# Performance work log

Hardware: AMD Instinct MI355X
Metric: run time of the kernel (lower is better)

The kernel has to match this reference:

```python
import jax, jax.numpy as jnp
import numpy as np

E = 1024   # embd_size
H = 16     # heads_num
DH = E // H
DFF = 4 * E
B, T = 2, 2048


def layer_norm(x, g, b, eps=1e-5):
    mu = jnp.mean(x, axis=-1, keepdims=True)
    var = jnp.var(x, axis=-1, keepdims=True)
    return (x - mu) * jax.lax.rsqrt(var + eps) * g + b


def setup_inputs() -> dict:
    key = jax.random.key(0)
    ks = jax.random.split(key, 12)
    s = 0.02
    return {
        "x": jax.random.normal(ks[0], (B, T, E), dtype=jnp.float32),
        "Wq": jax.random.normal(ks[1], (E, E), dtype=jnp.float32) * s,
        "Wk": jax.random.normal(ks[2], (E, E), dtype=jnp.float32) * s,
        "Wv": jax.random.normal(ks[3], (E, E), dtype=jnp.float32) * s,
        "Wo": jax.random.normal(ks[4], (E, E), dtype=jnp.float32) * s,
        "bo": jnp.zeros((E,), dtype=jnp.float32),
        "W1": jax.random.normal(ks[5], (E, DFF), dtype=jnp.float32) * s,
        "b1": jnp.zeros((DFF,), dtype=jnp.float32),
        "W2": jax.random.normal(ks[6], (DFF, E), dtype=jnp.float32) * s,
        "b2": jnp.zeros((E,), dtype=jnp.float32),
        "g1": jnp.ones((E,), dtype=jnp.float32),
        "be1": jnp.zeros((E,), dtype=jnp.float32),
        "g2": jnp.ones((E,), dtype=jnp.float32),
        "be2": jnp.zeros((E,), dtype=jnp.float32),
    }


def reference(x, Wq, Wk, Wv, Wo, bo, W1, b1, W2, b2, g1, be1, g2, be2):
    Bx, Tx, C = x.shape
    # --- self-attention sublayer ---
    h = layer_norm(x, g1, be1)
    # per-head projections; heads concatenated along output dim == stacked weights
    q = (h @ Wq).reshape(Bx, Tx, H, DH)  # [B,T,H,Dh]
    k = (h @ Wk).reshape(Bx, Tx, H, DH)
    v = (h @ Wv).reshape(Bx, Tx, H, DH)
    # NOTE: original scales by full embd_size**-0.5 (C = x.shape[-1]), not head_size
    scale = C ** (-0.5)
    scores = jnp.einsum("bqhd,bkhd->bhqk", q, k) * scale  # [B,H,T,T]
    mask = jnp.tril(jnp.ones((Tx, Tx), dtype=bool))
    scores = jnp.where(mask, scores, -jnp.inf)
    attn = jax.nn.softmax(scores, axis=-1)
    o = jnp.einsum("bhqk,bkhd->bqhd", attn, v).reshape(Bx, Tx, C)
    sa = o @ Wo + bo
    x = x + sa
    # --- feed-forward sublayer ---
    h2 = layer_norm(x, g2, be2)
    ff = jax.nn.relu(h2 @ W1 + b1) @ W2 + b2
    return x + ff
```

## Files before the change

### kernel.cpp

```cpp
#include <hip/hip_runtime.h>
#include <hip/hip_bf16.h>
#include <math.h>

#define Bn 2
#define Tn 2048
#define En 1024
#define Hn 16
#define DFFn 4096
#define Mn (Bn*Tn)
#define QKVLD 3072

typedef __hip_bfloat16 bf16;
typedef unsigned short u16;
typedef __attribute__((ext_vector_type(8))) short short8;
typedef __attribute__((ext_vector_type(4))) float f32x4;

typedef __attribute__((address_space(1))) const void cg_void;
typedef __attribute__((address_space(3))) void lds_void;

#define HBAR() asm volatile("s_waitcnt lgkmcnt(0)\n\ts_barrier" ::: "memory")

__device__ __forceinline__ u16 f2bf(float f) {
    bf16 h = __float2bfloat16(f);
    u16 u; __builtin_memcpy(&u, &h, 2); return u;
}

__global__ __launch_bounds__(256)
void transpose_w4(const float* __restrict__ s0, const float* __restrict__ s1,
                  const float* __restrict__ s2, const float* __restrict__ s3,
                  u16* __restrict__ d0, u16* __restrict__ d1,
                  u16* __restrict__ d2, u16* __restrict__ d3) {
    const float* src = (blockIdx.z == 0) ? s0 : (blockIdx.z == 1) ? s1
                     : (blockIdx.z == 2) ? s2 : s3;
    u16* dst = (blockIdx.z == 0) ? d0 : (blockIdx.z == 1) ? d1
             : (blockIdx.z == 2) ? d2 : d3;
    __shared__ float t[64][65];
    const int r0 = blockIdx.y * 64, c0 = blockIdx.x * 64;
    const int tr = threadIdx.x >> 6, tc = threadIdx.x & 63;
#pragma unroll
    for (int i = 0; i < 16; i++)
        t[tr + i * 4][tc] = src[(size_t)(r0 + tr + i * 4) * 1024 + c0 + tc];
    __syncthreads();
#pragma unroll
    for (int i = 0; i < 16; i++)
        dst[(size_t)(c0 + tr + i * 4) * 1024 + r0 + tc] = f2bf(t[tc][tr + i * 4]);
}

__global__ __launch_bounds__(256)
void transpose_w(const float* __restrict__ src, u16* __restrict__ dst,
                 int R, int C) {
    __shared__ float t[64][65];
    const int r0 = blockIdx.y * 64, c0 = blockIdx.x * 64;
    const int tr = threadIdx.x >> 6, tc = threadIdx.x & 63;
#pragma unroll
    for (int i = 0; i < 16; i++)
        t[tr + i * 4][tc] = src[(size_t)(r0 + tr + i * 4) * C + c0 + tc];
    __syncthreads();
#pragma unroll
    for (int i = 0; i < 16; i++)
        dst[(size_t)(c0 + tr + i * 4) * R + r0 + tc] = f2bf(t[tc][tr + i * 4]);
}

__global__ __launch_bounds__(256)
void ln_kernel(const float* __restrict__ x, const float* __restrict__ g,
               const float* __restrict__ b, u16* __restrict__ out) {
    const int row = blockIdx.x;
    const int tid = threadIdx.x;
    const float* xp = x + (size_t)row * En;
    float v[4];
    float s = 0.f, sq = 0.f;
#pragma unroll
    for (int i = 0; i < 4; i++) {
        v[i] = xp[tid + i * 256];
        s += v[i];
        sq += v[i] * v[i];
    }
    __shared__ float rs[256], rq[256];
    rs[tid] = s; rq[tid] = sq;
    __syncthreads();
    for (int st = 128; st > 0; st >>= 1) {
        if (tid < st) { rs[tid] += rs[tid + st]; rq[tid] += rq[tid + st]; }
        __syncthreads();
    }
    const float mu  = rs[0] * (1.0f / En);
    const float var = rq[0] * (1.0f / En) - mu * mu;
    const float inv = rsqrtf(var + 1e-5f);
#pragma unroll
    for (int i = 0; i < 4; i++) {
        const int c = tid + i * 256;
        out[(size_t)row * En + c] = f2bf((v[i] - mu) * inv * g[c] + b[c]);
    }
}

template<int TM, int HAS_BIAS, int RELU, int HAS_RES, int OUT_F32>
__global__ __launch_bounds__(256)
void gemm_bt(const u16* __restrict__ A, int ldA,
             const u16* __restrict__ Wt, int ldW,
             const float* __restrict__ bias, const float* __restrict__ res,
             void* __restrict__ Cout, int ldC, int Kd) {
    constexpr int IF = TM / 32;
    __shared__ __align__(16) u16 As[TM * 32];
    __shared__ __align__(16) u16 Bs[128 * 32];
    const int tid  = threadIdx.x;
    const int lane = tid & 63, wv = tid >> 6;
    const int quad = lane >> 4, l16 = lane & 15;
    const int m0 = blockIdx.y * TM, n0 = blockIdx.x * 128;
    const int rw = (wv >> 1) * (TM / 2), cw = (wv & 1) * 64;
    const int lr  = lane >> 2;
    const int gsw = ((lane & 3) ^ ((lane >> 3) & 3)) * 8;
    const int psw = (quad ^ ((l16 >> 1) & 3)) * 8;

    f32x4 acc[IF][4] = {};

    for (int kt = 0; kt < Kd; kt += 32) {
        __syncthreads();
#pragma unroll
        for (int t = 0; t < TM / 64; t++) {
            const int row = wv * (TM / 4) + t * 16;
            __builtin_amdgcn_global_load_lds(
                (cg_void*)(const void*)&A[(size_t)(m0 + row + lr) * ldA + kt + gsw],
                (lds_void*)(void*)&As[row * 32], 16, 0, 0);
        }
#pragma unroll
        for (int t = 0; t < 2; t++) {
            const int row = wv * 32 + t * 16;
            __builtin_amdgcn_global_load_lds(
                (cg_void*)(const void*)&Wt[(size_t)(n0 + row + lr) * ldW + kt + gsw],
                (lds_void*)(void*)&Bs[row * 32], 16, 0, 0);
        }
        __syncthreads();

        short8 af[IF], bfr[4];
#pragma unroll
        for (int i = 0; i < IF; i++)
            af[i] = *(const short8*)&As[(rw + i * 16 + l16) * 32 + psw];
#pragma unroll
        for (int j = 0; j < 4; j++)
            bfr[j] = *(const short8*)&Bs[(cw + j * 16 + l16) * 32 + psw];
#pragma unroll
        for (int i = 0; i < IF; i++)
#pragma unroll
            for (int j = 0; j < 4; j++)
                acc[i][j] = __builtin_amdgcn_mfma_f32_16x16x32_bf16(
                    af[i], bfr[j], acc[i][j], 0, 0, 0);
    }

#pragma unroll
    for (int i = 0; i < IF; i++) {
#pragma unroll
        for (int r = 0; r < 4; r++) {
            const int gm = m0 + rw + i * 16 + quad * 4 + r;
#pragma unroll
            for (int j = 0; j < 4; j++) {
                const int gn = n0 + cw + j * 16 + l16;
                float c = acc[i][j][r];
                if (HAS_BIAS) c += bias[gn];
                if (RELU) c = fmaxf(c, 0.f);
                if (HAS_RES) c += res[(size_t)gm * ldC + gn];
                if (OUT_F32) ((float*)Cout)[(size_t)gm * ldC + gn] = c;
                else         ((u16*)Cout)[(size_t)gm * ldC + gn] = f2bf(c);
            }
        }
    }
}

__global__ __launch_bounds__(256)
void flash_attn(u16* __restrict__ QKV) {
    const int hh = blockIdx.y, bb = blockIdx.z;
    const int tid  = threadIdx.x;
    const int lane = tid & 63, wv = tid >> 6;
    const int quad = lane >> 4, l16 = lane & 15;

    __shared__ __align__(16) u16 Qs[64 * 88];
    __shared__ __align__(16) u16 Ks[2][64 * 88];
    __shared__ __align__(16) u16 Vt[2][64 * 88];
    __shared__ __align__(16) u16 Ps[4][16 * 70];

    const size_t rowbase = (size_t)(bb * Tn) * QKVLD;
    const int sr = tid >> 2, scg = tid & 3;
    const int vkey = tid & 63, vw = tid >> 6;
    const float SC = 0.03125f * 1.44269504089f;

    for (int qsel = 0; qsel < 2; qsel++) {
        const int qt = qsel ? (31 - blockIdx.x) : blockIdx.x;

        HBAR();
        {
            const size_t qb = rowbase + (size_t)(qt * 64 + sr) * QKVLD + hh * 64;
            *(uint4*)&Qs[sr * 88 + scg * 8]       = *(const uint4*)&QKV[qb + scg * 8];
            *(uint4*)&Qs[sr * 88 + (scg + 4) * 8] = *(const uint4*)&QKV[qb + (scg + 4) * 8];
        }
        uint4 kreg0, kreg1, vreg0, vreg1;
        {
            const size_t kb = rowbase + (size_t)sr * QKVLD + 1024 + hh * 64;
            kreg0 = *(const uint4*)&QKV[kb + scg * 8];
            kreg1 = *(const uint4*)&QKV[kb + (scg + 4) * 8];
            const size_t vb = rowbase + (size_t)vkey * QKVLD + 2048 + hh * 64 + vw * 16;
            vreg0 = *(const uint4*)&QKV[vb];
            vreg1 = *(const uint4*)&QKV[vb + 8];
            *(uint4*)&Ks[0][sr * 88 + scg * 8]       = kreg0;
            *(uint4*)&Ks[0][sr * 88 + (scg + 4) * 8] = kreg1;
            u16 vtmp[16];
            *(uint4*)&vtmp[0] = vreg0;
            *(uint4*)&vtmp[8] = vreg1;
#pragma unroll
            for (int u = 0; u < 16; u++)
                Vt[0][(vw * 16 + u) * 88 + vkey] = vtmp[u];
        }
        if (qt >= 1) {
            const size_t kb = rowbase + (size_t)(64 + sr) * QKVLD + 1024 + hh * 64;
            kreg0 = *(const uint4*)&QKV[kb + scg * 8];
            kreg1 = *(const uint4*)&QKV[kb + (scg + 4) * 8];
            const size_t vb = rowbase + (size_t)(64 + vkey) * QKVLD + 2048 + hh * 64 + vw * 16;
            vreg0 = *(const uint4*)&QKV[vb];
            vreg1 = *(const uint4*)&QKV[vb + 8];
        }
        HBAR();
        short8 qf[2];
        qf[0] = *(const short8*)&Qs[(wv * 16 + l16) * 88 + quad * 8];
        qf[1] = *(const short8*)&Qs[(wv * 16 + l16) * 88 + 32 + quad * 8];

        f32x4 ot[4] = {};
        float m2 = -INFINITY, lrow = 0.f;

        for (int kt = 0; kt <= qt; kt++) {
            const int cur = kt & 1;

            f32x4 st[4] = {};
#pragma unroll
            for (int ks = 0; ks < 2; ks++)
#pragma unroll
                for (int i = 0; i < 4; i++) {
                    short8 kf = *(const short8*)&Ks[cur][(i * 16 + l16) * 88 + ks * 32 + quad * 8];
                    st[i] = __builtin_amdgcn_mfma_f32_16x16x32_bf16(kf, qf[ks], st[i], 0, 0, 0);
                }

            float p[4][4];
            float tmax = -INFINITY;
            if (kt == qt) {
                const int qloc = wv * 16 + l16;
#pragma unroll
                for (int i = 0; i < 4; i++)
#pragma unroll
                    for (int r = 0; r < 4; r++) {
                        float s = st[i][r] * SC;
                        if (i * 16 + quad * 4 + r > qloc) s = -INFINITY;
                        p[i][r] = s;
                        tmax = fmaxf(tmax, s);
                    }
            } else {
#pragma unroll
                for (int i = 0; i < 4; i++)
#pragma unroll
                    for (int r = 0; r < 4; r++) {
                        const float s = st[i][r] * SC;
                        p[i][r] = s;
                        tmax = fmaxf(tmax, s);
                    }
            }
            tmax = fmaxf(tmax, __shfl_xor(tmax, 16));
            tmax = fmaxf(tmax, __shfl_xor(tmax, 32));

            const float mnew = fmaxf(m2, tmax);
            const float alpha = exp2f(m2 - mnew);
            m2 = mnew;
            float psum = 0.f;
#pragma unroll
            for (int i = 0; i < 4; i++)
#pragma unroll
                for (int r = 0; r < 4; r++) {
                    const float e = exp2f(p[i][r] - mnew);
                    p[i][r] = e;
                    psum += e;
                }
            psum += __shfl_xor(psum, 16);
            psum += __shfl_xor(psum, 32);
            lrow = lrow * alpha + psum;
#pragma unroll
            for (int i = 0; i < 4; i++) ot[i] *= alpha;

#pragma unroll
            for (int i = 0; i < 4; i++)
#pragma unroll
                for (int r = 0; r < 4; r++)
                    Ps[wv][l16 * 70 + i * 16 + quad * 4 + r] = f2bf(p[i][r]);
            asm volatile("s_waitcnt lgkmcnt(0)" ::: "memory");

#pragma unroll
            for (int ks = 0; ks < 2; ks++) {
                short8 pf = *(const short8*)&Ps[wv][l16 * 70 + ks * 32 + quad * 8];
#pragma unroll
                for (int i = 0; i < 4; i++) {
                    short8 vf = *(const short8*)&Vt[cur][(i * 16 + l16) * 88 + ks * 32 + quad * 8];
                    ot[i] = __builtin_amdgcn_mfma_f32_16x16x32_bf16(vf, pf, ot[i], 0, 0, 0);
                }
            }

            if (kt < qt) {
                *(uint4*)&Ks[cur ^ 1][sr * 88 + scg * 8]       = kreg0;
                *(uint4*)&Ks[cur ^ 1][sr * 88 + (scg + 4) * 8] = kreg1;
                u16 vtmp[16];
                *(uint4*)&vtmp[0] = vreg0;
                *(uint4*)&vtmp[8] = vreg1;
#pragma unroll
                for (int u = 0; u < 16; u++)
                    Vt[cur ^ 1][(vw * 16 + u) * 88 + vkey] = vtmp[u];
                if (kt + 1 < qt) {
                    const size_t kb = rowbase + (size_t)((kt + 2) * 64 + sr) * QKVLD + 1024 + hh * 64;
                    kreg0 = *(const uint4*)&QKV[kb + scg * 8];
                    kreg1 = *(const uint4*)&QKV[kb + (scg + 4) * 8];
                    const size_t vb = rowbase + (size_t)((kt + 2) * 64 + vkey) * QKVLD + 2048 + hh * 64 + vw * 16;
                    vreg0 = *(const uint4*)&QKV[vb];
                    vreg1 = *(const uint4*)&QKV[vb + 8];
                }
                HBAR();
            }
        }

        const float linv = 1.0f / lrow;
        const size_t obase = rowbase + (size_t)(qt * 64 + wv * 16 + l16) * QKVLD + hh * 64;
#pragma unroll
        for (int i = 0; i < 4; i++) {
            ushort4 o4;
            o4.x = f2bf(ot[i][0] * linv);
            o4.y = f2bf(ot[i][1] * linv);
            o4.z = f2bf(ot[i][2] * linv);
            o4.w = f2bf(ot[i][3] * linv);
            *(ushort4*)&QKV[obase + i * 16 + quad * 4] = o4;
        }
    }
}

extern "C" void kernel_launch(void* const* d_in, const int* in_sizes, int n_in,
                              void* d_out, int out_size, void* d_ws, size_t ws_size,
                              hipStream_t stream) {
    const float* x   = (const float*)d_in[0];
    const float* Wq  = (const float*)d_in[1];
    const float* Wk  = (const float*)d_in[2];
    const float* Wv  = (const float*)d_in[3];
    const float* Wo  = (const float*)d_in[4];
    const float* bo  = (const float*)d_in[5];
    const float* W1  = (const float*)d_in[6];
    const float* b1  = (const float*)d_in[7];
    const float* W2  = (const float*)d_in[8];
    const float* b2  = (const float*)d_in[9];
    const float* g1  = (const float*)d_in[10];
    const float* be1 = (const float*)d_in[11];
    const float* g2  = (const float*)d_in[12];
    const float* be2 = (const float*)d_in[13];

    char* wsb = (char*)d_ws;
    u16*   QKV = (u16*)wsb;
    u16*   F1  = (u16*)wsb;
    u16*   W2T = (u16*)(wsb + 16u * 1024 * 1024);
    float* X1  = (float*)(wsb + 24u * 1024 * 1024);
    u16*   h     = (u16*)d_out;
    u16*   WT    = (u16*)((char*)d_out + 8u * 1024 * 1024);
    u16*   WqkvT = WT;
    u16*   WoT   = WT + 3u * 1024 * 1024;
    u16*   W1T   = WT;

    transpose_w4<<<dim3(16, 16, 4), 256, 0, stream>>>(
        Wq, Wk, Wv, Wo,
        WqkvT, WqkvT + 1024u * 1024, WqkvT + 2048u * 1024, WoT);

    ln_kernel<<<Mn, 256, 0, stream>>>(x, g1, be1, h);

    gemm_bt<128, 0, 0, 0, 0><<<dim3(24, 32), 256, 0, stream>>>(
        h, En, WqkvT, En, nullptr, nullptr, QKV, QKVLD, En);

    flash_attn<<<dim3(16, Hn, Bn), 256, 0, stream>>>(QKV);

    gemm_bt<64, 1, 0, 1, 1><<<dim3(8, 64), 256, 0, stream>>>(
        QKV, QKVLD, WoT, En, bo, x, X1, En, En);

    transpose_w<<<dim3(64, 16), 256, 0, stream>>>(W1, W1T, 1024, 4096);
    transpose_w<<<dim3(16, 64), 256, 0, stream>>>(W2, W2T, 4096, 1024);

    ln_kernel<<<Mn, 256, 0, stream>>>(X1, g2, be2, h);

    gemm_bt<128, 1, 1, 0, 0><<<dim3(16, 32), 256, 0, stream>>>(
        h, En, W1T, En, b1, nullptr, F1, 2048, En);
    gemm_bt<64, 0, 0, 1, 1><<<dim3(8, 64), 256, 0, stream>>>(
        F1, 2048, W2T, DFFn, nullptr, X1, X1, En, 2048);
    gemm_bt<128, 1, 1, 0, 0><<<dim3(16, 32), 256, 0, stream>>>(
        h, En, W1T + 2048u * 1024, En, b1 + 2048, nullptr, F1, 2048, En);
    gemm_bt<64, 1, 0, 1, 1><<<dim3(8, 64), 256, 0, stream>>>(
        F1, 2048, W2T + 2048, DFFn, b2, X1, (float*)d_out, En, 2048);
}
```

Baseline: 393.9 us.

## Use 128-key attention tiles and fold softmax scale into Q projection

The flash attention loop now processes 128 keys per round instead of 64, with a 64-key tail round for even query tiles. This halves the number of barriers and online-softmax rescales per query tile. Q fragments are loaded straight from global memory instead of being staged through LDS, and V is transposed with packed 32-bit LDS writes. The softmax scale times log2(e) is applied in the QKV GEMM epilogue before Q is rounded to bf16, which removes the per-score multiply but changes rounding slightly. Single buffering of K/V with register prefetch replaces the double-buffered LDS.

```diff
diff --git a/kernel.cpp b/kernel.cpp
--- a/kernel.cpp
+++ b/kernel.cpp
@@ -12,11 +12,14 @@
 
 typedef __hip_bfloat16 bf16;
 typedef unsigned short u16;
+typedef unsigned int u32;
 typedef __attribute__((ext_vector_type(8))) short short8;
 typedef __attribute__((ext_vector_type(4))) float f32x4;
 
 typedef __attribute__((address_space(1))) const void cg_void;
 typedef __attribute__((address_space(3))) void lds_void;
+
+#define QSC 0.0450842200278f
 
 #define HBAR() asm volatile("s_waitcnt lgkmcnt(0)\n\ts_barrier" ::: "memory")
 
@@ -92,7 +95,7 @@
     }
 }
 
-template<int TM, int HAS_BIAS, int RELU, int HAS_RES, int OUT_F32>
+template<int TM, int HAS_BIAS, int RELU, int HAS_RES, int OUT_F32, int SCQ>
 __global__ __launch_bounds__(256)
 void gemm_bt(const u16* __restrict__ A, int ldA,
              const u16* __restrict__ Wt, int ldW,
@@ -145,6 +148,7 @@
                     af[i], bfr[j], acc[i][j], 0, 0, 0);
     }
 
+    const float qscale = (SCQ && n0 < 1024) ? QSC : 1.0f;
 #pragma unroll
     for (int i = 0; i < IF; i++) {
 #pragma unroll
@@ -157,9 +161,73 @@
                 if (HAS_BIAS) c += bias[gn];
                 if (RELU) c = fmaxf(c, 0.f);
                 if (HAS_RES) c += res[(size_t)gm * ldC + gn];
+                if (SCQ) c *= qscale;
                 if (OUT_F32) ((float*)Cout)[(size_t)gm * ldC + gn] = c;
                 else         ((u16*)Cout)[(size_t)gm * ldC + gn] = f2bf(c);
             }
+        }
+    }
+}
+
+template<int NI, bool MASK>
+__device__ __forceinline__ void attn_round(
+    const u16* __restrict__ Ks, const u16* __restrict__ Vt,
+    u16* __restrict__ Psw, const short8* qf, f32x4* ot,
+    float& m2, float& lrow, int quad, int l16, int qloc) {
+    f32x4 st[NI];
+#pragma unroll
+    for (int i = 0; i < NI; i++) st[i] = (f32x4){0.f, 0.f, 0.f, 0.f};
+#pragma unroll
+    for (int ks = 0; ks < 2; ks++)
+#pragma unroll
+        for (int i = 0; i < NI; i++) {
+            short8 kf = *(const short8*)&Ks[(i * 16 + l16) * 72 + ks * 32 + quad * 8];
+            st[i] = __builtin_amdgcn_mfma_f32_16x16x32_bf16(kf, qf[ks], st[i], 0, 0, 0);
+        }
+    float tmax = -INFINITY;
+#pragma unroll
+    for (int i = 0; i < NI; i++)
+#pragma unroll
+        for (int r = 0; r < 4; r++) {
+            float s = st[i][r];
+            if (MASK && (i * 16 + quad * 4 + r > qloc)) s = -INFINITY;
+            st[i][r] = s;
+            tmax = fmaxf(tmax, s);
+        }
+    tmax = fmaxf(tmax, __shfl_xor(tmax, 16));
+    tmax = fmaxf(tmax, __shfl_xor(tmax, 32));
+    const float mnew = fmaxf(m2, tmax);
+    const float alpha = exp2f(m2 - mnew);
+    m2 = mnew;
+    float psum = 0.f;
+#pragma unroll
+    for (int i = 0; i < NI; i++)
+#pragma unroll
+        for (int r = 0; r < 4; r++) {
+            const float e = exp2f(st[i][r] - mnew);
+            st[i][r] = e;
+            psum += e;
+        }
+    psum += __shfl_xor(psum, 16);
+    psum += __shfl_xor(psum, 32);
+    lrow = lrow * alpha + psum;
+#pragma unroll
+    for (int i = 0; i < 4; i++) ot[i] *= alpha;
+#pragma unroll
+    for (int i = 0; i < NI; i++) {
+        uint2 w;
+        w.x = (u32)f2bf(st[i][0]) | ((u32)f2bf(st[i][1]) << 16);
+        w.y = (u32)f2bf(st[i][2]) | ((u32)f2bf(st[i][3]) << 16);
+        *(uint2*)&Psw[l16 * 136 + i * 16 + quad * 4] = w;
+    }
+    asm volatile("s_waitcnt lgkmcnt(0)" ::: "memory");
+#pragma unroll
+    for (int ks = 0; ks < NI / 2; ks++) {
+        short8 pf = *(const short8*)&Psw[l16 * 136 + ks * 32 + quad * 8];
+#pragma unroll
+        for (int i = 0; i < 4; i++) {
+            short8 vf = *(const short8*)&Vt[(i * 16 + l16) * 136 + ks * 32 + quad * 8];
+            ot[i] = __builtin_amdgcn_mfma_f32_16x16x32_bf16(vf, pf, ot[i], 0, 0, 0);
         }
     }
 }
@@ -171,154 +239,109 @@
     const int lane = tid & 63, wv = tid >> 6;
     const int quad = lane >> 4, l16 = lane & 15;
 
-    __shared__ __align__(16) u16 Qs[64 * 88];
-    __shared__ __align__(16) u16 Ks[2][64 * 88];
-    __shared__ __align__(16) u16 Vt[2][64 * 88];
-    __shared__ __align__(16) u16 Ps[4][16 * 70];
+    __shared__ __align__(16) u16 Ks[128 * 72];
+    __shared__ __align__(16) u16 Vt[64 * 136];
+    __shared__ __align__(16) u16 Ps[4][16 * 136];
 
     const size_t rowbase = (size_t)(bb * Tn) * QKVLD;
-    const int sr = tid >> 2, scg = tid & 3;
-    const int vkey = tid & 63, vw = tid >> 6;
-    const float SC = 0.03125f * 1.44269504089f;
+    const int k_r = tid >> 1, k_g = tid & 1;
+    const int v_kk = (tid & 63) * 2, v_dh = wv * 16;
+    const int k64_r = tid >> 2, k64_g = tid & 3;
+    const int v64_kk = (tid & 31) * 2, v64_dh = (tid >> 5) * 8;
+
+    uint4 kr0, kr1, kr2, kr3, vr0, vr1, vr2, vr3;
+
+    auto prefetch128 = [&](int kb) {
+        const size_t kbb = rowbase + (size_t)(kb + k_r) * QKVLD + 1024 + hh * 64;
+        kr0 = *(const uint4*)&QKV[kbb + k_g * 8];
+        kr1 = *(const uint4*)&QKV[kbb + (k_g + 2) * 8];
+        kr2 = *(const uint4*)&QKV[kbb + (k_g + 4) * 8];
+        kr3 = *(const uint4*)&QKV[kbb + (k_g + 6) * 8];
+        const size_t vb0 = rowbase + (size_t)(kb + v_kk) * QKVLD + 2048 + hh * 64 + v_dh;
+        vr0 = *(const uint4*)&QKV[vb0];
+        vr1 = *(const uint4*)&QKV[vb0 + 8];
+        vr2 = *(const uint4*)&QKV[vb0 + QKVLD];
+        vr3 = *(const uint4*)&QKV[vb0 + QKVLD + 8];
+    };
+    auto write128 = [&]() {
+        *(uint4*)&Ks[k_r * 72 + k_g * 8]       = kr0;
+        *(uint4*)&Ks[k_r * 72 + (k_g + 2) * 8] = kr1;
+        *(uint4*)&Ks[k_r * 72 + (k_g + 4) * 8] = kr2;
+        *(uint4*)&Ks[k_r * 72 + (k_g + 6) * 8] = kr3;
+        u16 va[16], vb[16];
+        *(uint4*)&va[0] = vr0; *(uint4*)&va[8] = vr1;
+        *(uint4*)&vb[0] = vr2; *(uint4*)&vb[8] = vr3;
+#pragma unroll
+        for (int j = 0; j < 16; j++) {
+            const u32 w = (u32)va[j] | ((u32)vb[j] << 16);
+            *(u32*)&Vt[(v_dh + j) * 136 + v_kk] = w;
+        }
+    };
+    auto stage64 = [&](int kb) {
+        const size_t kbb = rowbase + (size_t)(kb + k64_r) * QKVLD + 1024 + hh * 64;
+        *(uint4*)&Ks[k64_r * 72 + k64_g * 8]       = *(const uint4*)&QKV[kbb + k64_g * 8];
+        *(uint4*)&Ks[k64_r * 72 + (k64_g + 4) * 8] = *(const uint4*)&QKV[kbb + (k64_g + 4) * 8];
+        const size_t vb0 = rowbase + (size_t)(kb + v64_kk) * QKVLD + 2048 + hh * 64 + v64_dh;
+        uint4 p0 = *(const uint4*)&QKV[vb0];
+        uint4 p1 = *(const uint4*)&QKV[vb0 + QKVLD];
+        u16 pa[8], pb[8];
+        *(uint4*)&pa[0] = p0; *(uint4*)&pb[0] = p1;
+#pragma unroll
+        for (int j = 0; j < 8; j++) {
+            const u32 w = (u32)pa[j] | ((u32)pb[j] << 16);
+            *(u32*)&Vt[(v64_dh + j) * 136 + v64_kk] = w;
+        }
+    };
 
     for (int qsel = 0; qsel < 2; qsel++) {
         const int qt = qsel ? (31 - blockIdx.x) : blockIdx.x;
-
-        HBAR();
-        {
-            const size_t qb = rowbase + (size_t)(qt * 64 + sr) * QKVLD + hh * 64;
-            *(uint4*)&Qs[sr * 88 + scg * 8]       = *(const uint4*)&QKV[qb + scg * 8];
-            *(uint4*)&Qs[sr * 88 + (scg + 4) * 8] = *(const uint4*)&QKV[qb + (scg + 4) * 8];
-        }
-        uint4 kreg0, kreg1, vreg0, vreg1;
-        {
-            const size_t kb = rowbase + (size_t)sr * QKVLD + 1024 + hh * 64;
-            kreg0 = *(const uint4*)&QKV[kb + scg * 8];
-            kreg1 = *(const uint4*)&QKV[kb + (scg + 4) * 8];
-            const size_t vb = rowbase + (size_t)vkey * QKVLD + 2048 + hh * 64 + vw * 16;
-            vreg0 = *(const uint4*)&QKV[vb];
-            vreg1 = *(const uint4*)&QKV[vb + 8];
-            *(uint4*)&Ks[0][sr * 88 + scg * 8]       = kreg0;
-            *(uint4*)&Ks[0][sr * 88 + (scg + 4) * 8] = kreg1;
-            u16 vtmp[16];
-            *(uint4*)&vtmp[0] = vreg0;
-            *(uint4*)&vtmp[8] = vreg1;
-#pragma unroll
-            for (int u = 0; u < 16; u++)
-                Vt[0][(vw * 16 + u) * 88 + vkey] = vtmp[u];
-        }
-        if (qt >= 1) {
-            const size_t kb = rowbase + (size_t)(64 + sr) * QKVLD + 1024 + hh * 64;
-            kreg0 = *(const uint4*)&QKV[kb + scg * 8];
-            kreg1 = *(const uint4*)&QKV[kb + (scg + 4) * 8];
-            const size_t vb = rowbase + (size_t)(64 + vkey) * QKVLD + 2048 + hh * 64 + vw * 16;
-            vreg0 = *(const uint4*)&QKV[vb];
-            vreg1 = *(const uint4*)&QKV[vb + 8];
-        }
-        HBAR();
+        const int n128 = (qt >> 1) + (qt & 1);
+        const int qloc16 = wv * 16 + l16;
+
+        const size_t qrow = rowbase + (size_t)(qt * 64 + qloc16) * QKVLD + hh * 64;
         short8 qf[2];
-        qf[0] = *(const short8*)&Qs[(wv * 16 + l16) * 88 + quad * 8];
-        qf[1] = *(const short8*)&Qs[(wv * 16 + l16) * 88 + 32 + quad * 8];
+        qf[0] = *(const short8*)&QKV[qrow + quad * 8];
+        qf[1] = *(const short8*)&QKV[qrow + 32 + quad * 8];
 
         f32x4 ot[4] = {};
         float m2 = -INFINITY, lrow = 0.f;
 
-        for (int kt = 0; kt <= qt; kt++) {
-            const int cur = kt & 1;
-
-            f32x4 st[4] = {};
-#pragma unroll
-            for (int ks = 0; ks < 2; ks++)
-#pragma unroll
-                for (int i = 0; i < 4; i++) {
-                    short8 kf = *(const short8*)&Ks[cur][(i * 16 + l16) * 88 + ks * 32 + quad * 8];
-                    st[i] = __builtin_amdgcn_mfma_f32_16x16x32_bf16(kf, qf[ks], st[i], 0, 0, 0);
-                }
-
-            float p[4][4];
-            float tmax = -INFINITY;
-            if (kt == qt) {
-                const int qloc = wv * 16 + l16;
-#pragma unroll
-                for (int i = 0; i < 4; i++)
-#pragma unroll
-                    for (int r = 0; r < 4; r++) {
-                        float s = st[i][r] * SC;
-                        if (i * 16 + quad * 4 + r > qloc) s = -INFINITY;
-                        p[i][r] = s;
-                        tmax = fmaxf(tmax, s);
-                    }
-            } else {
-#pragma unroll
-                for (int i = 0; i < 4; i++)
-#pragma unroll
-                    for (int r = 0; r < 4; r++) {
-                        const float s = st[i][r] * SC;
-                        p[i][r] = s;
-                        tmax = fmaxf(tmax, s);
-                    }
-            }
-            tmax = fmaxf(tmax, __shfl_xor(tmax, 16));
-            tmax = fmaxf(tmax, __shfl_xor(tmax, 32));
-
-            const float mnew = fmaxf(m2, tmax);
-            const float alpha = exp2f(m2 - mnew);
-            m2 = mnew;
-            float psum = 0.f;
-#pragma unroll
-            for (int i = 0; i < 4; i++)
-#pragma unroll
-                for (int r = 0; r < 4; r++) {
-                    const float e = exp2f(p[i][r] - mnew);
-                    p[i][r] = e;
-                    psum += e;
-                }
-            psum += __shfl_xor(psum, 16);
-            psum += __shfl_xor(psum, 32);
-            lrow = lrow * alpha + psum;
-#pragma unroll
-            for (int i = 0; i < 4; i++) ot[i] *= alpha;
-
-#pragma unroll
-            for (int i = 0; i < 4; i++)
-#pragma unroll
-                for (int r = 0; r < 4; r++)
-                    Ps[wv][l16 * 70 + i * 16 + quad * 4 + r] = f2bf(p[i][r]);
-            asm volatile("s_waitcnt lgkmcnt(0)" ::: "memory");
-
-#pragma unroll
-            for (int ks = 0; ks < 2; ks++) {
-                short8 pf = *(const short8*)&Ps[wv][l16 * 70 + ks * 32 + quad * 8];
-#pragma unroll
-                for (int i = 0; i < 4; i++) {
-                    short8 vf = *(const short8*)&Vt[cur][(i * 16 + l16) * 88 + ks * 32 + quad * 8];
-                    ot[i] = __builtin_amdgcn_mfma_f32_16x16x32_bf16(vf, pf, ot[i], 0, 0, 0);
+        HBAR();
+        if (n128 > 0) {
+            prefetch128(0);
+            write128();
+            if (n128 > 1) prefetch128(128);
+            HBAR();
+            for (int f = 0; f < n128; f++) {
+                const bool maskthis = (qt & 1) && (f == n128 - 1);
+                if (maskthis)
+                    attn_round<8, true>(Ks, Vt, &Ps[wv][0], qf, ot, m2, lrow,
+                                        quad, l16, qloc16 + 64);
+                else
+                    attn_round<8, false>(Ks, Vt, &Ps[wv][0], qf, ot, m2, lrow,
+                                         quad, l16, 0);
+                HBAR();
+                if (f + 1 < n128) {
+                    write128();
+                    if (f + 2 < n128) prefetch128((f + 2) * 128);
+                    HBAR();
+                } else if (!(qt & 1)) {
+                    stage64(qt * 64);
+                    HBAR();
                 }
             }
-
-            if (kt < qt) {
-                *(uint4*)&Ks[cur ^ 1][sr * 88 + scg * 8]       = kreg0;
-                *(uint4*)&Ks[cur ^ 1][sr * 88 + (scg + 4) * 8] = kreg1;
-                u16 vtmp[16];
-                *(uint4*)&vtmp[0] = vreg0;
-                *(uint4*)&vtmp[8] = vreg1;
-#pragma unroll
-                for (int u = 0; u < 16; u++)
-                    Vt[cur ^ 1][(vw * 16 + u) * 88 + vkey] = vtmp[u];
-                if (kt + 1 < qt) {
-                    const size_t kb = rowbase + (size_t)((kt + 2) * 64 + sr) * QKVLD + 1024 + hh * 64;
-                    kreg0 = *(const uint4*)&QKV[kb + scg * 8];
-                    kreg1 = *(const uint4*)&QKV[kb + (scg + 4) * 8];
-                    const size_t vb = rowbase + (size_t)((kt + 2) * 64 + vkey) * QKVLD + 2048 + hh * 64 + vw * 16;
-                    vreg0 = *(const uint4*)&QKV[vb];
-                    vreg1 = *(const uint4*)&QKV[vb + 8];
-                }
-                HBAR();
-            }
+            if (!(qt & 1))
+                attn_round<4, true>(Ks, Vt, &Ps[wv][0], qf, ot, m2, lrow,
+                                    quad, l16, qloc16);
+        } else {
+            stage64(0);
+            HBAR();
+            attn_round<4, true>(Ks, Vt, &Ps[wv][0], qf, ot, m2, lrow,
+                                quad, l16, qloc16);
         }
 
         const float linv = 1.0f / lrow;
-        const size_t obase = rowbase + (size_t)(qt * 64 + wv * 16 + l16) * QKVLD + hh * 64;
+        const size_t obase = rowbase + (size_t)(qt * 64 + qloc16) * QKVLD + hh * 64;
 #pragma unroll
         for (int i = 0; i < 4; i++) {
             ushort4 o4;
@@ -366,12 +389,12 @@
 
     ln_kernel<<<Mn, 256, 0, stream>>>(x, g1, be1, h);
 
-    gemm_bt<128, 0, 0, 0, 0><<<dim3(24, 32), 256, 0, stream>>>(
+    gemm_bt<128, 0, 0, 0, 0, 1><<<dim3(24, 32), 256, 0, stream>>>(
         h, En, WqkvT, En, nullptr, nullptr, QKV, QKVLD, En);
 
     flash_attn<<<dim3(16, Hn, Bn), 256, 0, stream>>>(QKV);
 
-    gemm_bt<64, 1, 0, 1, 1><<<dim3(8, 64), 256, 0, stream>>>(
+    gemm_bt<64, 1, 0, 1, 1, 0><<<dim3(8, 64), 256, 0, stream>>>(
         QKV, QKVLD, WoT, En, bo, x, X1, En, En);
 
     transpose_w<<<dim3(64, 16), 256, 0, stream>>>(W1, W1T, 1024, 4096);
@@ -379,12 +402,12 @@
 
     ln_kernel<<<Mn, 256, 0, stream>>>(X1, g2, be2, h);
 
-    gemm_bt<128, 1, 1, 0, 0><<<dim3(16, 32), 256, 0, stream>>>(
+    gemm_bt<128, 1, 1, 0, 0, 0><<<dim3(16, 32), 256, 0, stream>>>(
         h, En, W1T, En, b1, nullptr, F1, 2048, En);
-    gemm_bt<64, 0, 0, 1, 1><<<dim3(8, 64), 256, 0, stream>>>(
+    gemm_bt<64, 0, 0, 1, 1, 0><<<dim3(8, 64), 256, 0, stream>>>(
         F1, 2048, W2T, DFFn, nullptr, X1, X1, En, 2048);
-    gemm_bt<128, 1, 1, 0, 0><<<dim3(16, 32), 256, 0, stream>>>(
+    gemm_bt<128, 1, 1, 0, 0, 0><<<dim3(16, 32), 256, 0, stream>>>(
         h, En, W1T + 2048u * 1024, En, b1 + 2048, nullptr, F1, 2048, En);
-    gemm_bt<64, 1, 0, 1, 1><<<dim3(8, 64), 256, 0, stream>>>(
+    gemm_bt<64, 1, 0, 1, 1, 0><<<dim3(8, 64), 256, 0, stream>>>(
         F1, 2048, W2T + 2048, DFFn, b2, X1, (float*)d_out, En, 2048);
 }
```

Result: no change. 399.8 us (+1.5%).

## Split causal attention across two KV halves with merge pass and pre-transposed V

Applied to the files above, without the earlier changes.

Splits each query tile's key range into two interleaved halves handled by separate blocks, doubling the attention grid, and merges the partial outputs in a new kernel using saved max and sum statistics. V is pre-transposed into a separate buffer by a new kernel, so flash blocks load it with vector loads instead of scalar LDS transposes. LDS tiles use XOR swizzling instead of padding, and the softmax scale is folded into the Q projection epilogue. The residual X1 is also stored as bf16 instead of fp32 to cut traffic. These add extra kernel launches and bf16 rounding of partial outputs and the residual, which may cost accuracy.

```diff
diff --git a/kernel.cpp b/kernel.cpp
--- a/kernel.cpp
+++ b/kernel.cpp
@@ -12,17 +12,23 @@
 
 typedef __hip_bfloat16 bf16;
 typedef unsigned short u16;
+typedef unsigned int u32;
 typedef __attribute__((ext_vector_type(8))) short short8;
 typedef __attribute__((ext_vector_type(4))) float f32x4;
 
 typedef __attribute__((address_space(1))) const void cg_void;
 typedef __attribute__((address_space(3))) void lds_void;
+
+#define QSC 0.0450842200278f
 
 #define HBAR() asm volatile("s_waitcnt lgkmcnt(0)\n\ts_barrier" ::: "memory")
 
 __device__ __forceinline__ u16 f2bf(float f) {
     bf16 h = __float2bfloat16(f);
     u16 u; __builtin_memcpy(&u, &h, 2); return u;
+}
+__device__ __forceinline__ float bf2f(u16 u) {
+    u32 x = ((u32)u) << 16; float f; __builtin_memcpy(&f, &x, 4); return f;
 }
 
 __global__ __launch_bounds__(256)
@@ -62,16 +68,35 @@
 }
 
 __global__ __launch_bounds__(256)
-void ln_kernel(const float* __restrict__ x, const float* __restrict__ g,
+void vcopy_t(const u16* __restrict__ QKV, u16* __restrict__ Vg) {
+    const int bh = blockIdx.z;
+    const int t0 = blockIdx.y * 64;
+    __shared__ u16 t[64][65];
+    const int tr = threadIdx.x >> 6, tc = threadIdx.x & 63;
+    const u16* src = QKV + (size_t)(bh >> 4) * 2048 * QKVLD + 2048 + (bh & 15) * 64;
+#pragma unroll
+    for (int i = 0; i < 16; i++)
+        t[tr + i * 4][tc] = src[(size_t)(t0 + tr + i * 4) * QKVLD + tc];
+    __syncthreads();
+    u16* dst = Vg + (size_t)bh * 64 * 2048;
+#pragma unroll
+    for (int i = 0; i < 16; i++)
+        dst[(size_t)(tr + i * 4) * 2048 + t0 + tc] = t[tc][tr + i * 4];
+}
+
+template<typename AT>
+__global__ __launch_bounds__(256)
+void ln_kernel(const AT* __restrict__ x, const float* __restrict__ g,
                const float* __restrict__ b, u16* __restrict__ out) {
     const int row = blockIdx.x;
     const int tid = threadIdx.x;
-    const float* xp = x + (size_t)row * En;
+    const AT* xp = x + (size_t)row * En;
     float v[4];
     float s = 0.f, sq = 0.f;
 #pragma unroll
     for (int i = 0; i < 4; i++) {
-        v[i] = xp[tid + i * 256];
+        if constexpr (sizeof(AT) == 2) v[i] = bf2f(xp[tid + i * 256]);
+        else                           v[i] = (float)xp[tid + i * 256];
         s += v[i];
         sq += v[i] * v[i];
     }
@@ -92,11 +117,11 @@
     }
 }
 
-template<int TM, int HAS_BIAS, int RELU, int HAS_RES, int OUT_F32>
+template<int TM, int HAS_BIAS, int RELU, int RES, int OUT_F32, int SCQ>
 __global__ __launch_bounds__(256)
 void gemm_bt(const u16* __restrict__ A, int ldA,
              const u16* __restrict__ Wt, int ldW,
-             const float* __restrict__ bias, const float* __restrict__ res,
+             const float* __restrict__ bias, const void* __restrict__ res,
              void* __restrict__ Cout, int ldC, int Kd) {
     constexpr int IF = TM / 32;
     __shared__ __align__(16) u16 As[TM * 32];
@@ -145,6 +170,7 @@
                     af[i], bfr[j], acc[i][j], 0, 0, 0);
     }
 
+    const float qscale = (SCQ && n0 < 1024) ? QSC : 1.0f;
 #pragma unroll
     for (int i = 0; i < IF; i++) {
 #pragma unroll
@@ -156,7 +182,9 @@
                 float c = acc[i][j][r];
                 if (HAS_BIAS) c += bias[gn];
                 if (RELU) c = fmaxf(c, 0.f);
-                if (HAS_RES) c += res[(size_t)gm * ldC + gn];
+                if (RES == 1) c += ((const float*)res)[(size_t)gm * ldC + gn];
+                if (RES == 2) c += bf2f(((const u16*)res)[(size_t)gm * ldC + gn]);
+                if (SCQ) c *= qscale;
                 if (OUT_F32) ((float*)Cout)[(size_t)gm * ldC + gn] = c;
                 else         ((u16*)Cout)[(size_t)gm * ldC + gn] = f2bf(c);
             }
@@ -165,170 +193,199 @@
 }
 
 __global__ __launch_bounds__(256)
-void flash_attn(u16* __restrict__ QKV) {
+void flash_pass1(const u16* __restrict__ QKV, const u16* __restrict__ Vg,
+                 u16* __restrict__ Op0, u16* __restrict__ Op1qkv,
+                 float* __restrict__ stats) {
+    const int pr = blockIdx.x >> 1, half = blockIdx.x & 1;
     const int hh = blockIdx.y, bb = blockIdx.z;
     const int tid  = threadIdx.x;
     const int lane = tid & 63, wv = tid >> 6;
     const int quad = lane >> 4, l16 = lane & 15;
 
-    __shared__ __align__(16) u16 Qs[64 * 88];
-    __shared__ __align__(16) u16 Ks[2][64 * 88];
-    __shared__ __align__(16) u16 Vt[2][64 * 88];
-    __shared__ __align__(16) u16 Ps[4][16 * 70];
+    __shared__ __align__(16) u16 Ks[2][64 * 64];
+    __shared__ __align__(16) u16 Vt[2][64 * 64];
+    __shared__ __align__(16) u16 Ps[4][16 * 64];
 
     const size_t rowbase = (size_t)(bb * Tn) * QKVLD;
-    const int sr = tid >> 2, scg = tid & 3;
-    const int vkey = tid & 63, vw = tid >> 6;
-    const float SC = 0.03125f * 1.44269504089f;
+    const u16* Vgh = Vg + (size_t)(bb * Hn + hh) * 64 * 2048;
+
+    const int sr = tid >> 2;
+    const int p0 = (tid & 3) | ((sr & 1) << 2);
+    const int p1 = p0 ^ 4;
+    const int g0 = p0 ^ (sr & 7), g1 = p1 ^ (sr & 7);
+    const int lsw = l16 & 7;
+
+    uint4 kA, kB, vA, vB;
+    auto prefetch = [&](int kt) {
+        const size_t kb = rowbase + (size_t)(kt * 64 + sr) * QKVLD + 1024 + hh * 64;
+        kA = *(const uint4*)&QKV[kb + g0 * 8];
+        kB = *(const uint4*)&QKV[kb + g1 * 8];
+        const size_t vb = (size_t)sr * 2048 + kt * 64;
+        vA = *(const uint4*)&Vgh[vb + g0 * 8];
+        vB = *(const uint4*)&Vgh[vb + g1 * 8];
+    };
+    auto writebuf = [&](int buf) {
+        *(uint4*)&Ks[buf][sr * 64 + p0 * 8] = kA;
+        *(uint4*)&Ks[buf][sr * 64 + p1 * 8] = kB;
+        *(uint4*)&Vt[buf][sr * 64 + p0 * 8] = vA;
+        *(uint4*)&Vt[buf][sr * 64 + p1 * 8] = vB;
+    };
 
     for (int qsel = 0; qsel < 2; qsel++) {
-        const int qt = qsel ? (31 - blockIdx.x) : blockIdx.x;
-
-        HBAR();
-        {
-            const size_t qb = rowbase + (size_t)(qt * 64 + sr) * QKVLD + hh * 64;
-            *(uint4*)&Qs[sr * 88 + scg * 8]       = *(const uint4*)&QKV[qb + scg * 8];
-            *(uint4*)&Qs[sr * 88 + (scg + 4) * 8] = *(const uint4*)&QKV[qb + (scg + 4) * 8];
-        }
-        uint4 kreg0, kreg1, vreg0, vreg1;
-        {
-            const size_t kb = rowbase + (size_t)sr * QKVLD + 1024 + hh * 64;
-            kreg0 = *(const uint4*)&QKV[kb + scg * 8];
-            kreg1 = *(const uint4*)&QKV[kb + (scg + 4) * 8];
-            const size_t vb = rowbase + (size_t)vkey * QKVLD + 2048 + hh * 64 + vw * 16;
-            vreg0 = *(const uint4*)&QKV[vb];
-            vreg1 = *(const uint4*)&QKV[vb + 8];
-            *(uint4*)&Ks[0][sr * 88 + scg * 8]       = kreg0;
-            *(uint4*)&Ks[0][sr * 88 + (scg + 4) * 8] = kreg1;
-            u16 vtmp[16];
-            *(uint4*)&vtmp[0] = vreg0;
-            *(uint4*)&vtmp[8] = vreg1;
-#pragma unroll
-            for (int u = 0; u < 16; u++)
-                Vt[0][(vw * 16 + u) * 88 + vkey] = vtmp[u];
-        }
-        if (qt >= 1) {
-            const size_t kb = rowbase + (size_t)(64 + sr) * QKVLD + 1024 + hh * 64;
-            kreg0 = *(const uint4*)&QKV[kb + scg * 8];
-            kreg1 = *(const uint4*)&QKV[kb + (scg + 4) * 8];
-            const size_t vb = rowbase + (size_t)(64 + vkey) * QKVLD + 2048 + hh * 64 + vw * 16;
-            vreg0 = *(const uint4*)&QKV[vb];
-            vreg1 = *(const uint4*)&QKV[vb + 8];
-        }
-        HBAR();
-        short8 qf[2];
-        qf[0] = *(const short8*)&Qs[(wv * 16 + l16) * 88 + quad * 8];
-        qf[1] = *(const short8*)&Qs[(wv * 16 + l16) * 88 + 32 + quad * 8];
+        const int qt = qsel ? (31 - pr) : pr;
+        const int nk = (qt >= half) ? ((qt - half) >> 1) + 1 : 0;
+        const int qrow = qt * 64 + wv * 16 + l16;
+        const int grow = bb * Tn + qrow;
 
         f32x4 ot[4] = {};
         float m2 = -INFINITY, lrow = 0.f;
 
-        for (int kt = 0; kt <= qt; kt++) {
-            const int cur = kt & 1;
-
-            f32x4 st[4] = {};
-#pragma unroll
-            for (int ks = 0; ks < 2; ks++)
+        HBAR();
+        if (nk > 0) {
+            const u16* qp = QKV + rowbase + (size_t)qrow * QKVLD + hh * 64;
+            short8 qf[2];
+            qf[0] = *(const short8*)&qp[quad * 8];
+            qf[1] = *(const short8*)&qp[32 + quad * 8];
+
+            prefetch(half);
+            writebuf(0);
+            if (nk > 1) prefetch(half + 2);
+            HBAR();
+
+            const bool hasdiag = ((qt ^ half) & 1) == 0;
+            for (int f = 0; f < nk; f++) {
+                const int cur = f & 1;
+
+                f32x4 st[4] = {};
+#pragma unroll
+                for (int ks = 0; ks < 2; ks++)
+#pragma unroll
+                    for (int i = 0; i < 4; i++) {
+                        short8 kf = *(const short8*)&Ks[cur][(i * 16 + l16) * 64 +
+                                     (((ks * 4 + quad) ^ lsw) * 8)];
+                        st[i] = __builtin_amdgcn_mfma_f32_16x16x32_bf16(
+                            kf, qf[ks], st[i], 0, 0, 0);
+                    }
+
+                float tmax = -INFINITY;
+                if (hasdiag && f == nk - 1) {
+                    const int qloc = wv * 16 + l16;
+#pragma unroll
+                    for (int i = 0; i < 4; i++)
+#pragma unroll
+                        for (int r = 0; r < 4; r++) {
+                            float s = st[i][r];
+                            if (i * 16 + quad * 4 + r > qloc) s = -INFINITY;
+                            st[i][r] = s;
+                            tmax = fmaxf(tmax, s);
+                        }
+                } else {
+#pragma unroll
+                    for (int i = 0; i < 4; i++)
+#pragma unroll
+                        for (int r = 0; r < 4; r++)
+                            tmax = fmaxf(tmax, st[i][r]);
+                }
+                tmax = fmaxf(tmax, __shfl_xor(tmax, 16));
+                tmax = fmaxf(tmax, __shfl_xor(tmax, 32));
+
+                const float mnew = fmaxf(m2, tmax);
+                const float alpha = exp2f(m2 - mnew);
+                m2 = mnew;
+                float psum = 0.f;
+#pragma unroll
+                for (int i = 0; i < 4; i++)
+#pragma unroll
+                    for (int r = 0; r < 4; r++) {
+                        const float e = exp2f(st[i][r] - mnew);
+                        st[i][r] = e;
+                        psum += e;
+                    }
+                psum += __shfl_xor(psum, 16);
+                psum += __shfl_xor(psum, 32);
+                lrow = lrow * alpha + psum;
+#pragma unroll
+                for (int i = 0; i < 4; i++) ot[i] *= alpha;
+
 #pragma unroll
                 for (int i = 0; i < 4; i++) {
-                    short8 kf = *(const short8*)&Ks[cur][(i * 16 + l16) * 88 + ks * 32 + quad * 8];
-                    st[i] = __builtin_amdgcn_mfma_f32_16x16x32_bf16(kf, qf[ks], st[i], 0, 0, 0);
+                    uint2 w;
+                    w.x = (u32)f2bf(st[i][0]) | ((u32)f2bf(st[i][1]) << 16);
+                    w.y = (u32)f2bf(st[i][2]) | ((u32)f2bf(st[i][3]) << 16);
+                    const int g = (i * 2 + (quad >> 1)) ^ lsw;
+                    *(uint2*)&Ps[wv][l16 * 64 + g * 8 + (quad & 1) * 4] = w;
                 }
-
-            float p[4][4];
-            float tmax = -INFINITY;
-            if (kt == qt) {
-                const int qloc = wv * 16 + l16;
-#pragma unroll
-                for (int i = 0; i < 4; i++)
-#pragma unroll
-                    for (int r = 0; r < 4; r++) {
-                        float s = st[i][r] * SC;
-                        if (i * 16 + quad * 4 + r > qloc) s = -INFINITY;
-                        p[i][r] = s;
-                        tmax = fmaxf(tmax, s);
+                asm volatile("s_waitcnt lgkmcnt(0)" ::: "memory");
+
+#pragma unroll
+                for (int ks = 0; ks < 2; ks++) {
+                    short8 pf = *(const short8*)&Ps[wv][l16 * 64 +
+                                 (((ks * 4 + quad) ^ lsw) * 8)];
+#pragma unroll
+                    for (int i = 0; i < 4; i++) {
+                        short8 vf = *(const short8*)&Vt[cur][(i * 16 + l16) * 64 +
+                                     (((ks * 4 + quad) ^ lsw) * 8)];
+                        ot[i] = __builtin_amdgcn_mfma_f32_16x16x32_bf16(
+                            vf, pf, ot[i], 0, 0, 0);
                     }
-            } else {
-#pragma unroll
-                for (int i = 0; i < 4; i++)
-#pragma unroll
-                    for (int r = 0; r < 4; r++) {
-                        const float s = st[i][r] * SC;
-                        p[i][r] = s;
-                        tmax = fmaxf(tmax, s);
-                    }
-            }
-            tmax = fmaxf(tmax, __shfl_xor(tmax, 16));
-            tmax = fmaxf(tmax, __shfl_xor(tmax, 32));
-
-            const float mnew = fmaxf(m2, tmax);
-            const float alpha = exp2f(m2 - mnew);
-            m2 = mnew;
-            float psum = 0.f;
-#pragma unroll
-            for (int i = 0; i < 4; i++)
-#pragma unroll
-                for (int r = 0; r < 4; r++) {
-                    const float e = exp2f(p[i][r] - mnew);
-                    p[i][r] = e;
-                    psum += e;
                 }
-            psum += __shfl_xor(psum, 16);
-            psum += __shfl_xor(psum, 32);
-            lrow = lrow * alpha + psum;
-#pragma unroll
-            for (int i = 0; i < 4; i++) ot[i] *= alpha;
-
-#pragma unroll
-            for (int i = 0; i < 4; i++)
-#pragma unroll
-                for (int r = 0; r < 4; r++)
-                    Ps[wv][l16 * 70 + i * 16 + quad * 4 + r] = f2bf(p[i][r]);
-            asm volatile("s_waitcnt lgkmcnt(0)" ::: "memory");
-
-#pragma unroll
-            for (int ks = 0; ks < 2; ks++) {
-                short8 pf = *(const short8*)&Ps[wv][l16 * 70 + ks * 32 + quad * 8];
-#pragma unroll
-                for (int i = 0; i < 4; i++) {
-                    short8 vf = *(const short8*)&Vt[cur][(i * 16 + l16) * 88 + ks * 32 + quad * 8];
-                    ot[i] = __builtin_amdgcn_mfma_f32_16x16x32_bf16(vf, pf, ot[i], 0, 0, 0);
+
+                if (f + 1 < nk) {
+                    writebuf(cur ^ 1);
+                    if (f + 2 < nk) prefetch(half + 2 * (f + 2));
+                    HBAR();
                 }
             }
-
-            if (kt < qt) {
-                *(uint4*)&Ks[cur ^ 1][sr * 88 + scg * 8]       = kreg0;
-                *(uint4*)&Ks[cur ^ 1][sr * 88 + (scg + 4) * 8] = kreg1;
-                u16 vtmp[16];
-                *(uint4*)&vtmp[0] = vreg0;
-                *(uint4*)&vtmp[8] = vreg1;
-#pragma unroll
-                for (int u = 0; u < 16; u++)
-                    Vt[cur ^ 1][(vw * 16 + u) * 88 + vkey] = vtmp[u];
-                if (kt + 1 < qt) {
-                    const size_t kb = rowbase + (size_t)((kt + 2) * 64 + sr) * QKVLD + 1024 + hh * 64;
-                    kreg0 = *(const uint4*)&QKV[kb + scg * 8];
-                    kreg1 = *(const uint4*)&QKV[kb + (scg + 4) * 8];
-                    const size_t vb = rowbase + (size_t)((kt + 2) * 64 + vkey) * QKVLD + 2048 + hh * 64 + vw * 16;
-                    vreg0 = *(const uint4*)&QKV[vb];
-                    vreg1 = *(const uint4*)&QKV[vb + 8];
-                }
-                HBAR();
+        }
+
+        if (half == 0) {
+            u16* op = Op0 + (size_t)grow * 1024 + hh * 64;
+#pragma unroll
+            for (int i = 0; i < 4; i++) {
+                ushort4 o4;
+                o4.x = f2bf(ot[i][0]); o4.y = f2bf(ot[i][1]);
+                o4.z = f2bf(ot[i][2]); o4.w = f2bf(ot[i][3]);
+                *(ushort4*)&op[i * 16 + quad * 4] = o4;
             }
-        }
-
-        const float linv = 1.0f / lrow;
-        const size_t obase = rowbase + (size_t)(qt * 64 + wv * 16 + l16) * QKVLD + hh * 64;
-#pragma unroll
-        for (int i = 0; i < 4; i++) {
-            ushort4 o4;
-            o4.x = f2bf(ot[i][0] * linv);
-            o4.y = f2bf(ot[i][1] * linv);
-            o4.z = f2bf(ot[i][2] * linv);
-            o4.w = f2bf(ot[i][3] * linv);
-            *(ushort4*)&QKV[obase + i * 16 + quad * 4] = o4;
-        }
-    }
+        } else {
+            u16* op = Op1qkv + (size_t)grow * QKVLD + 2048 + hh * 64;
+#pragma unroll
+            for (int i = 0; i < 4; i++) {
+                ushort4 o4;
+                o4.x = f2bf(ot[i][0]); o4.y = f2bf(ot[i][1]);
+                o4.z = f2bf(ot[i][2]); o4.w = f2bf(ot[i][3]);
+                *(ushort4*)&op[i * 16 + quad * 4] = o4;
+            }
+        }
+        if (quad == 0) {
+            stats[((size_t)(half * 2 + 0) * 4096 + grow) * 16 + hh] = m2;
+            stats[((size_t)(half * 2 + 1) * 4096 + grow) * 16 + hh] = lrow;
+        }
+    }
+}
+
+__global__ __launch_bounds__(256)
+void flash_merge(u16* __restrict__ QKV, const u16* __restrict__ Op0,
+                 const float* __restrict__ stats) {
+    const int row = blockIdx.x;
+    const int tid = threadIdx.x;
+    const int col = tid * 4;
+    const int hh = col >> 6;
+    const float m0 = stats[((size_t)0 * 4096 + row) * 16 + hh];
+    const float l0 = stats[((size_t)1 * 4096 + row) * 16 + hh];
+    const float m1 = stats[((size_t)2 * 4096 + row) * 16 + hh];
+    const float l1 = stats[((size_t)3 * 4096 + row) * 16 + hh];
+    const float m  = fmaxf(m0, m1);
+    const float w0 = exp2f(m0 - m), w1 = exp2f(m1 - m);
+    const float inv = 1.0f / (w0 * l0 + w1 * l1);
+    ushort4 a = *(const ushort4*)&Op0[(size_t)row * 1024 + col];
+    ushort4 b = *(const ushort4*)&QKV[(size_t)row * QKVLD + 2048 + col];
+    ushort4 o;
+    o.x = f2bf((w0 * bf2f(a.x) + w1 * bf2f(b.x)) * inv);
+    o.y = f2bf((w0 * bf2f(a.y) + w1 * bf2f(b.y)) * inv);
+    o.z = f2bf((w0 * bf2f(a.z) + w1 * bf2f(b.z)) * inv);
+    o.w = f2bf((w0 * bf2f(a.w) + w1 * bf2f(b.w)) * inv);
+    *(ushort4*)&QKV[(size_t)row * QKVLD + col] = o;
 }
 
 extern "C" void kernel_launch(void* const* d_in, const int* in_sizes, int n_in,
@@ -353,38 +410,45 @@
     u16*   QKV = (u16*)wsb;
     u16*   F1  = (u16*)wsb;
     u16*   W2T = (u16*)(wsb + 16u * 1024 * 1024);
-    float* X1  = (float*)(wsb + 24u * 1024 * 1024);
+    u16*   Op0 = (u16*)(wsb + 24u * 1024 * 1024);
+    u16*   X1b = Op0;
+    u16*   Vg  = (u16*)(wsb + 32u * 1024 * 1024);
     u16*   h     = (u16*)d_out;
     u16*   WT    = (u16*)((char*)d_out + 8u * 1024 * 1024);
     u16*   WqkvT = WT;
     u16*   WoT   = WT + 3u * 1024 * 1024;
+    float* stats = (float*)WT;
     u16*   W1T   = WT;
 
     transpose_w4<<<dim3(16, 16, 4), 256, 0, stream>>>(
         Wq, Wk, Wv, Wo,
         WqkvT, WqkvT + 1024u * 1024, WqkvT + 2048u * 1024, WoT);
 
-    ln_kernel<<<Mn, 256, 0, stream>>>(x, g1, be1, h);
-
-    gemm_bt<128, 0, 0, 0, 0><<<dim3(24, 32), 256, 0, stream>>>(
+    ln_kernel<float><<<Mn, 256, 0, stream>>>(x, g1, be1, h);
+
+    gemm_bt<128, 0, 0, 0, 0, 1><<<dim3(24, 32), 256, 0, stream>>>(
         h, En, WqkvT, En, nullptr, nullptr, QKV, QKVLD, En);
 
-    flash_attn<<<dim3(16, Hn, Bn), 256, 0, stream>>>(QKV);
-
-    gemm_bt<64, 1, 0, 1, 1><<<dim3(8, 64), 256, 0, stream>>>(
-        QKV, QKVLD, WoT, En, bo, x, X1, En, En);
+    vcopy_t<<<dim3(1, 32, 32), 256, 0, stream>>>(QKV, Vg);
+
+    flash_pass1<<<dim3(32, Hn, Bn), 256, 0, stream>>>(QKV, Vg, Op0, QKV, stats);
+
+    flash_merge<<<Mn, 256, 0, stream>>>(QKV, Op0, stats);
+
+    gemm_bt<64, 1, 0, 1, 0, 0><<<dim3(8, 64), 256, 0, stream>>>(
+        QKV, QKVLD, WoT, En, bo, x, X1b, En, En);
 
     transpose_w<<<dim3(64, 16), 256, 0, stream>>>(W1, W1T, 1024, 4096);
     transpose_w<<<dim3(16, 64), 256, 0, stream>>>(W2, W2T, 4096, 1024);
 
-    ln_kernel<<<Mn, 256, 0, stream>>>(X1, g2, be2, h);
-
-    gemm_bt<128, 1, 1, 0, 0><<<dim3(16, 32), 256, 0, stream>>>(
+    ln_kernel<u16><<<Mn, 256, 0, stream>>>(X1b, g2, be2, h);
+
+    gemm_bt<128, 1, 1, 0, 0, 0><<<dim3(16, 32), 256, 0, stream>>>(
         h, En, W1T, En, b1, nullptr, F1, 2048, En);
-    gemm_bt<64, 0, 0, 1, 1><<<dim3(8, 64), 256, 0, stream>>>(
-        F1, 2048, W2T, DFFn, nullptr, X1, X1, En, 2048);
-    gemm_bt<128, 1, 1, 0, 0><<<dim3(16, 32), 256, 0, stream>>>(
+    gemm_bt<64, 0, 0, 2, 0, 0><<<dim3(8, 64), 256, 0, stream>>>(
+        F1, 2048, W2T, DFFn, nullptr, X1b, X1b, En, 2048);
+    gemm_bt<128, 1, 1, 0, 0, 0><<<dim3(16, 32), 256, 0, stream>>>(
         h, En, W1T + 2048u * 1024, En, b1 + 2048, nullptr, F1, 2048, En);
-    gemm_bt<64, 1, 0, 1, 1><<<dim3(8, 64), 256, 0, stream>>>(
-        F1, 2048, W2T + 2048, DFFn, b2, X1, (float*)d_out, En, 2048);
-}
+    gemm_bt<64, 1, 0, 2, 1, 0><<<dim3(8, 64), 256, 0, stream>>>(
+        F1, 2048, W2T + 2048, DFFn, b2, X1b, (float*)d_out, En, 2048);
+}
```

Result: no change. 392.1 us (-0.5%).
